# Performance work log

Measured on AMD Instinct MI355X. Metric: run time of the kernel, lower is better.

## Reference

```python
import jax, jax.numpy as jnp
import numpy as np

N_NODES = 50000
N_EDGES = 800000
N_RELS = 20
N_BASES = 8


def setup_inputs() -> dict:
    key = jax.random.key(0)
    ks = jax.random.split(key, 12)
    s = 0.05  # keep activations well-scaled through summed messages
    return {
        "src": jax.random.randint(ks[0], (N_EDGES,), 0, N_NODES),
        "dst": jax.random.randint(ks[1], (N_EDGES,), 0, N_NODES),
        "etype": jax.random.randint(ks[2], (N_EDGES,), 0, N_RELS),
        "num_nodes": N_NODES,
        "basis0": jax.random.normal(ks[3], (N_BASES, 1, 128), jnp.float32) * s,
        "wcomp0": jax.random.normal(ks[4], (N_RELS, N_BASES), jnp.float32),
        "bias0": jax.random.normal(ks[5], (128,), jnp.float32) * s,
        "basis1": jax.random.normal(ks[6], (N_BASES, 128, 128), jnp.float32) * s,
        "wcomp1": jax.random.normal(ks[7], (N_RELS, N_BASES), jnp.float32),
        "bias1": jax.random.normal(ks[8], (128,), jnp.float32) * s,
        "lin_w": jax.random.normal(ks[9], (128, 64), jnp.float32) * s,
        "lin_b": jax.random.normal(ks[10], (64,), jnp.float32) * s,
    }


def _relgraphconv(h, basis, w_comp, bias, src, dst, etype, num_nodes, relu):
    # Basis decomposition: W[r] = sum_b w_comp[r,b] * basis[b]  -> [R, in, out]
    W = jnp.einsum("rb,bio->rio", w_comp, basis)
    # Project every node under every relation once: [N, R, out]
    proj = jnp.einsum("ni,rio->nro", h, W)
    # Per-edge message = h[src] @ W[etype]  (gather, irregular access)
    msg = proj[src, etype]                       # [E, out]
    # Sum-aggregate messages into destination nodes (DGL fn.sum)
    agg = jax.ops.segment_sum(msg, dst, num_segments=num_nodes)
    out = agg + bias
    return jax.nn.relu(out) if relu else out


def reference(src, dst, etype, num_nodes, basis0, wcomp0, bias0,
              basis1, wcomp1, bias1, lin_w, lin_b):
    # Embedder.forward: h starts as ones [N, 1]
    h = jnp.ones((num_nodes, 1), jnp.float32)
    h = _relgraphconv(h, basis0, wcomp0, bias0, src, dst, etype, num_nodes, True)
    h = _relgraphconv(h, basis1, wcomp1, bias1, src, dst, etype, num_nodes, True)
    # conv_output=False -> final layer is plain Linear
    return h @ lin_w + lin_b
```

## Files before the change

### kernel.cpp

```cpp
#include <hip/hip_runtime.h>
#include <hip/hip_bf16.h>

#define NN 50000
#define NE 800000
#define NR 20
#define NB 8
#define D  128
#define DO 64
#define NT 782
#define NBKT (NT*1280)
#define NSB 978

typedef __attribute__((ext_vector_type(8))) short short8;
typedef __attribute__((ext_vector_type(4))) float f32x4;

__device__ inline unsigned short f2bf(float f) {
    __hip_bfloat16 h = __float2bfloat16(f);
    return *reinterpret_cast<unsigned short*>(&h);
}
__device__ inline float bf2f(unsigned short u) {
    unsigned x = ((unsigned)u) << 16;
    float f;
    __builtin_memcpy(&f, &x, 4);
    return f;
}


__global__ __launch_bounds__(1024) void k_wh(
        const int* __restrict__ dst, const int* __restrict__ et,
        const float* __restrict__ basis0, const float* __restrict__ wcomp0,
        const float* __restrict__ basis1, const float* __restrict__ wcomp1,
        const float* __restrict__ lin_w,
        int* __restrict__ cnt2, float* __restrict__ W0,
        unsigned short* __restrict__ W1b, unsigned short* __restrict__ linWb) {
    int b = blockIdx.x;
    if (b < NT) {
        int i = b * 1024 + threadIdx.x;
        if (i < NE) {
            int d = dst[i];
            int key = (d >> 6) * 1280 + et[i] * 64 + (d & 63);
            atomicAdd(&cnt2[key], 1);
        }
        return;
    }
    int idx = (b - NT) * 1024 + threadIdx.x;
    if (idx < NR * D) {
        int r = idx / D, o = idx % D;
        float a = 0.f;
        #pragma unroll
        for (int bb = 0; bb < NB; bb++) a += wcomp0[r * NB + bb] * basis0[bb * D + o];
        W0[idx] = a;
    }
    if (idx < 16 * 64) {
        int lane = idx & 63, fr = idx >> 6;
        int kc = fr >> 2, nt = fr & 3;
        int i0 = kc * 32 + (lane >> 4) * 8;
        int o = nt * 16 + (lane & 15);
        short8 v;
        #pragma unroll
        for (int e = 0; e < 8; e++) v[e] = (short)f2bf(lin_w[(i0 + e) * DO + o]);
        *((short8*)linWb + idx) = v;
    }
    if (idx < NR * 4 * 8 * 64) {
        int lane = idx & 63;
        int cb   = (idx >> 6) & 7;
        int kc   = (idx >> 9) & 3;
        int rel  = idx >> 11;
        float wc[NB];
        #pragma unroll
        for (int bb = 0; bb < NB; bb++) wc[bb] = wcomp1[rel * NB + bb];
        int o  = cb * 16 + (lane & 15);
        int i0 = kc * 32 + (lane >> 4) * 8;
        short8 v;
        #pragma unroll
        for (int e = 0; e < 8; e++) {
            int i = i0 + e;
            float a = 0.f;
            #pragma unroll
            for (int bb = 0; bb < NB; bb++) a += wc[bb] * basis1[(bb * D + i) * D + o];
            v[e] = (short)f2bf(a);
        }
        *((short8*)W1b + idx) = v;
    }
}

__global__ __launch_bounds__(1024) void k_scan1(const int* __restrict__ cnt2,
                                                int* __restrict__ boff2,
                                                int* __restrict__ bsum) {
    __shared__ int ws[16];
    int t = threadIdx.x, lane = t & 63, wv = t >> 6;
    int i = blockIdx.x * 1024 + t;
    int v = (i < NBKT) ? cnt2[i] : 0;
    int inc = v;
    for (int dd = 1; dd < 64; dd <<= 1) {
        int u = __shfl_up(inc, dd);
        if (lane >= dd) inc += u;
    }
    if (lane == 63) ws[wv] = inc;
    __syncthreads();
    if (t == 0) { int a = 0; for (int j = 0; j < 16; j++) { int x = ws[j]; ws[j] = a; a += x; } }
    __syncthreads();
    int ex = ws[wv] + inc - v;
    if (i < NBKT) boff2[i] = ex;
    if (t == 1023) bsum[blockIdx.x] = ex + v;
}

__global__ __launch_bounds__(1024) void k_scan2(int* __restrict__ bsum) {
    __shared__ int ws[16];
    int t = threadIdx.x, lane = t & 63, wv = t >> 6;
    int v = (t < NSB) ? bsum[t] : 0;
    int inc = v;
    for (int dd = 1; dd < 64; dd <<= 1) {
        int u = __shfl_up(inc, dd);
        if (lane >= dd) inc += u;
    }
    if (lane == 63) ws[wv] = inc;
    __syncthreads();
    if (t == 0) { int a = 0; for (int j = 0; j < 16; j++) { int x = ws[j]; ws[j] = a; a += x; } }
    __syncthreads();
    if (t < NSB) bsum[t] = ws[wv] + inc - v;
}

__global__ __launch_bounds__(1024) void k_scan3(int* __restrict__ boff2,
                                                const int* __restrict__ bsum,
                                                int* __restrict__ gcur2) {
    int i = blockIdx.x * 1024 + threadIdx.x;
    if (i < NBKT) {
        int f = boff2[i] + bsum[i >> 10];
        boff2[i] = f;
        gcur2[i] = f;
    }
    if (i == 0) boff2[NBKT] = NE;
}

__global__ __launch_bounds__(1024) void k_sh(
        const int* __restrict__ src, const int* __restrict__ dst,
        const int* __restrict__ et, int* __restrict__ gcur2,
        unsigned short* __restrict__ epack,
        const int* __restrict__ cnt2, const float* __restrict__ W0,
        const float* __restrict__ bias0, unsigned short* __restrict__ h1b) {
    int b = blockIdx.x, t = threadIdx.x;
    if (b < NT) {
        int i = b * 1024 + t;
        if (i < NE) {
            int d = dst[i];
            int key = (d >> 6) * 1280 + et[i] * 64 + (d & 63);
            int pos = atomicAdd(&gcur2[key], 1);
            epack[pos] = (unsigned short)src[i];
        }
        return;
    }
    __shared__ float cs[NR * 64];
    __shared__ float w0s[NR * D];
    int tile = b - NT;
    for (int j = t; j < NR * 64; j += 1024) cs[j] = (float)cnt2[tile * 1280 + j];
    for (int j = t; j < NR * D; j += 1024) w0s[j] = W0[j];
    __syncthreads();
    int nl = t >> 4, cg = t & 15;
    int n = tile * 64 + nl;
    if (n < NN) {
        float a[8];
        #pragma unroll
        for (int j = 0; j < 8; j++) a[j] = bias0[cg * 8 + j];
        for (int r = 0; r < NR; r++) {
            float c = cs[r * 64 + nl];
            #pragma unroll
            for (int j = 0; j < 8; j++) a[j] += c * w0s[r * D + cg * 8 + j];
        }
        short8 o;
        #pragma unroll
        for (int j = 0; j < 8; j++) o[j] = (short)f2bf(fmaxf(a[j], 0.f));
        *((short8*)(h1b + n * D + cg * 8)) = o;
    }
}

__global__ __launch_bounds__(512, 2) void k_mega(
        const unsigned short* __restrict__ epack, const int* __restrict__ boff2,
        const unsigned short* __restrict__ h1b,
        const unsigned short* __restrict__ W1b,
        const unsigned short* __restrict__ linWb,
        const float* __restrict__ bias1, const float* __restrict__ lin_b,
        float* __restrict__ out) {
    __shared__ __align__(16) char lds[17408 + 16384];
    __shared__ unsigned short ooffs[1282];
    __shared__ unsigned short epk[2048];

    short8* Raw8 = (short8*)lds;
    short8* Sl8  = (short8*)(lds + 17408);

    int t = threadIdx.x, tile = blockIdx.x;
    int wv = t >> 6, lane = t & 63;
    int le = t >> 3, lp = t & 7;
    int dl = t >> 3, cg = t & 7;
    int row = lane & 15, gg = lane >> 4;

    int kbase = tile * 1280;
    int tb = boff2[kbase];
    for (int i = t; i < 1281; i += 512)
        ooffs[i] = (unsigned short)(boff2[kbase + i] - tb);
    __syncthreads();
    int nE = min((int)ooffs[1280], 2048);
    for (int i = t; i < nE; i += 512) epk[i] = epack[tb + i];
    __syncthreads();

    f32x4 acc[4];
    #pragma unroll
    for (int j = 0; j < 4; j++) acc[j] = (f32x4){0.f, 0.f, 0.f, 0.f};

    for (int r = 0; r < NR; r++) {
        int rbase = ooffs[r * 64];
        int cnt = ooffs[r * 64 + 64] - rbase;
        if (cnt == 0) continue;

        const short8* Wg8 = (const short8*)W1b + r * 2048;
        short8 breg[4];
        #pragma unroll
        for (int kc = 0; kc < 4; kc++) breg[kc] = Wg8[(kc * 8 + wv) * 64 + lane];

        float s[16];
        #pragma unroll
        for (int k = 0; k < 16; k++) s[k] = 0.f;
        int o0 = ooffs[r * 64 + dl] - rbase;
        int o1 = ooffs[r * 64 + dl + 1] - rbase;
        int nc = (cnt + 63) >> 6;

        for (int c = 0; c < nc; c++) {
            int cb0 = c * 64, m = min(64, cnt - cb0);
            if (c > 0) __syncthreads();
            if (le < m) {
                int node = epk[rbase + cb0 + le];
                const short8* hp = (const short8*)(h1b + (size_t)node * D) + lp * 2;
                Raw8[le * 17 + lp * 2]     = hp[0];
                Raw8[le * 17 + lp * 2 + 1] = hp[1];
            }
            __syncthreads();
            int lo = max(o0 - cb0, 0), hi = min(o1 - cb0, m);
            for (int p = lo; p < hi; p++) {
                short8 w0 = Raw8[p * 17 + 2 * cg];
                short8 w1 = Raw8[p * 17 + 2 * cg + 1];
                #pragma unroll
                for (int k = 0; k < 8; k++) {
                    s[k]     += bf2f((unsigned short)w0[k]);
                    s[8 + k] += bf2f((unsigned short)w1[k]);
                }
            }
        }
        short8 p0, p1;
        #pragma unroll
        for (int k = 0; k < 8; k++) {
            p0[k] = (short)f2bf(s[k]);
            p1[k] = (short)f2bf(s[8 + k]);
        }
        Sl8[dl * 16 + ((cg * 2)     ^ (dl & 15))] = p0;
        Sl8[dl * 16 + ((cg * 2 + 1) ^ (dl & 15))] = p1;
        __syncthreads();
        #pragma unroll
        for (int rb = 0; rb < 4; rb++) {
            int arow = rb * 16 + row;
            #pragma unroll
            for (int kc = 0; kc < 4; kc++) {
                short8 a = Sl8[arow * 16 + ((kc * 4 + gg) ^ (arow & 15))];
                acc[rb] = __builtin_amdgcn_mfma_f32_16x16x32_bf16(a, breg[kc], acc[rb], 0, 0, 0);
            }
        }
    }

    __syncthreads();
    unsigned short* Af = (unsigned short*)lds;
    #pragma unroll
    for (int rb = 0; rb < 4; rb++) {
        #pragma unroll
        for (int reg = 0; reg < 4; reg++) {
            int rr = rb * 16 + gg * 4 + reg;
            int col = wv * 16 + row;
            Af[rr * 136 + col] = f2bf(fmaxf(acc[rb][reg] + bias1[col], 0.f));
        }
    }
    __syncthreads();
    {
        int rb = wv & 3;
        int nt0 = (wv >> 2) * 2, nt1 = nt0 + 1;
        f32x4 ao0 = (f32x4){0.f, 0.f, 0.f, 0.f};
        f32x4 ao1 = (f32x4){0.f, 0.f, 0.f, 0.f};
        #pragma unroll
        for (int kc = 0; kc < 4; kc++) {
            short8 a = *(const short8*)(Af + (rb * 16 + row) * 136 + kc * 32 + gg * 8);
            short8 b0 = *((const short8*)linWb + (kc * 4 + nt0) * 64 + lane);
            short8 b1 = *((const short8*)linWb + (kc * 4 + nt1) * 64 + lane);
            ao0 = __builtin_amdgcn_mfma_f32_16x16x32_bf16(a, b0, ao0, 0, 0, 0);
            ao1 = __builtin_amdgcn_mfma_f32_16x16x32_bf16(a, b1, ao1, 0, 0, 0);
        }
        float lb0 = lin_b[nt0 * 16 + row];
        float lb1 = lin_b[nt1 * 16 + row];
        #pragma unroll
        for (int reg = 0; reg < 4; reg++) {
            int d = tile * 64 + rb * 16 + gg * 4 + reg;
            if (d < NN) {
                out[d * DO + nt0 * 16 + row] = ao0[reg] + lb0;
                out[d * DO + nt1 * 16 + row] = ao1[reg] + lb1;
            }
        }
    }
}

extern "C" void kernel_launch(void* const* d_in, const int* in_sizes, int n_in,
                              void* d_out, int out_size, void* d_ws, size_t ws_size,
                              hipStream_t stream) {
    const int*   src    = (const int*)d_in[0];
    const int*   dst    = (const int*)d_in[1];
    const int*   et     = (const int*)d_in[2];
    const float* basis0 = (const float*)d_in[4];
    const float* wcomp0 = (const float*)d_in[5];
    const float* bias0  = (const float*)d_in[6];
    const float* basis1 = (const float*)d_in[7];
    const float* wcomp1 = (const float*)d_in[8];
    const float* bias1  = (const float*)d_in[9];
    const float* lin_w  = (const float*)d_in[10];
    const float* lin_b  = (const float*)d_in[11];
    float* out = (float*)d_out;

    char* ws = (char*)d_ws;
    int*            cnt2    = (int*)           (ws + 0);
    int*            bsum    = (int*)           (ws + 4003840);
    int*            boff2   = (int*)           (ws + 4007808);
    int*            gcur2   = (int*)           (ws + 8011712);
    float*          W0      = (float*)         (ws + 12015616);
    unsigned short* W1b     = (unsigned short*)(ws + 12025856);
    unsigned short* h1b     = (unsigned short*)(ws + 12681216);
    unsigned short* epack   = (unsigned short*)(ws + 25481216);
    unsigned short* linWb   = (unsigned short*)(ws + 28681216);

    hipMemsetAsync(ws, 0, 4003840, stream);

    k_wh<<<NT + 40, 1024, 0, stream>>>(dst, et, basis0, wcomp0, basis1, wcomp1,
                                       lin_w, cnt2, W0, W1b, linWb);
    k_scan1<<<NSB, 1024, 0, stream>>>(cnt2, boff2, bsum);
    k_scan2<<<1, 1024, 0, stream>>>(bsum);
    k_scan3<<<NSB, 1024, 0, stream>>>(boff2, bsum, gcur2);
    k_sh<<<NT * 2, 1024, 0, stream>>>(src, dst, et, gcur2, epack,
                                      cnt2, W0, bias0, h1b);
    k_mega<<<NT, 512, 0, stream>>>(epack, boff2, h1b, W1b, linWb,
                                   bias1, lin_b, out);
}
```

Before: 190.0 us.

## Replace fine-grained global bucket scan with coarse tile-relation scan plus in-LDS sub-sort

The global counting sort now buckets edges by (dst tile, relation) instead of (dst tile, relation, dst lane). This shrinks the scan to a single-block kernel and drops two scan launches. Each edge packs relation, local dst and src into one int, and the mega kernel re-sorts its tile's edges in LDS using per-tile counts and local atomics. The aim is to cut scan work, kernel launches and the memset size, at the cost of extra LDS atomics, a per-block local scan, and 4-byte rather than 2-byte edge records.

```diff
diff --git a/kernel.cpp b/kernel.cpp
--- a/kernel.cpp
+++ b/kernel.cpp
@@ -8,8 +8,7 @@
 #define D  128
 #define DO 64
 #define NT 782
-#define NBKT (NT*1280)
-#define NSB 978
+#define NRB (NT*NR)
 
 typedef __attribute__((ext_vector_type(8))) short short8;
 typedef __attribute__((ext_vector_type(4))) float f32x4;
@@ -31,15 +30,16 @@
         const float* __restrict__ basis0, const float* __restrict__ wcomp0,
         const float* __restrict__ basis1, const float* __restrict__ wcomp1,
         const float* __restrict__ lin_w,
-        int* __restrict__ cnt2, float* __restrict__ W0,
-        unsigned short* __restrict__ W1b, unsigned short* __restrict__ linWb) {
+        int* __restrict__ cnt2, int* __restrict__ cntR,
+        float* __restrict__ W0, unsigned short* __restrict__ W1b,
+        unsigned short* __restrict__ linWb) {
     int b = blockIdx.x;
     if (b < NT) {
         int i = b * 1024 + threadIdx.x;
         if (i < NE) {
-            int d = dst[i];
-            int key = (d >> 6) * 1280 + et[i] * 64 + (d & 63);
-            atomicAdd(&cnt2[key], 1);
+            int d = dst[i], e = et[i];
+            atomicAdd(&cnt2[(d >> 6) * 1280 + e * 64 + (d & 63)], 1);
+            atomicAdd(&cntR[(d >> 6) * NR + e], 1);
         }
         return;
     }
@@ -84,69 +84,50 @@
     }
 }
 
-__global__ __launch_bounds__(1024) void k_scan1(const int* __restrict__ cnt2,
-                                                int* __restrict__ boff2,
-                                                int* __restrict__ bsum) {
+__global__ __launch_bounds__(1024) void k_scanR(const int* __restrict__ cntR,
+                                                int* __restrict__ boffR,
+                                                int* __restrict__ gcurR) {
     __shared__ int ws[16];
     int t = threadIdx.x, lane = t & 63, wv = t >> 6;
-    int i = blockIdx.x * 1024 + t;
-    int v = (i < NBKT) ? cnt2[i] : 0;
-    int inc = v;
+    int v[16]; int s = 0;
+    #pragma unroll
+    for (int j = 0; j < 16; j++) {
+        int idx = t * 16 + j;
+        v[j] = (idx < NRB) ? cntR[idx] : 0;
+        s += v[j];
+    }
+    int inc = s;
     for (int dd = 1; dd < 64; dd <<= 1) {
         int u = __shfl_up(inc, dd);
         if (lane >= dd) inc += u;
     }
     if (lane == 63) ws[wv] = inc;
     __syncthreads();
-    if (t == 0) { int a = 0; for (int j = 0; j < 16; j++) { int x = ws[j]; ws[j] = a; a += x; } }
-    __syncthreads();
-    int ex = ws[wv] + inc - v;
-    if (i < NBKT) boff2[i] = ex;
-    if (t == 1023) bsum[blockIdx.x] = ex + v;
-}
-
-__global__ __launch_bounds__(1024) void k_scan2(int* __restrict__ bsum) {
-    __shared__ int ws[16];
-    int t = threadIdx.x, lane = t & 63, wv = t >> 6;
-    int v = (t < NSB) ? bsum[t] : 0;
-    int inc = v;
-    for (int dd = 1; dd < 64; dd <<= 1) {
-        int u = __shfl_up(inc, dd);
-        if (lane >= dd) inc += u;
-    }
-    if (lane == 63) ws[wv] = inc;
-    __syncthreads();
-    if (t == 0) { int a = 0; for (int j = 0; j < 16; j++) { int x = ws[j]; ws[j] = a; a += x; } }
-    __syncthreads();
-    if (t < NSB) bsum[t] = ws[wv] + inc - v;
-}
-
-__global__ __launch_bounds__(1024) void k_scan3(int* __restrict__ boff2,
-                                                const int* __restrict__ bsum,
-                                                int* __restrict__ gcur2) {
-    int i = blockIdx.x * 1024 + threadIdx.x;
-    if (i < NBKT) {
-        int f = boff2[i] + bsum[i >> 10];
-        boff2[i] = f;
-        gcur2[i] = f;
-    }
-    if (i == 0) boff2[NBKT] = NE;
+    if (t == 0) { int a = 0; for (int i = 0; i < 16; i++) { int x = ws[i]; ws[i] = a; a += x; } }
+    __syncthreads();
+    int base = ws[wv] + inc - s;
+    #pragma unroll
+    for (int j = 0; j < 16; j++) {
+        int idx = t * 16 + j;
+        if (idx < NRB) { boffR[idx] = base; gcurR[idx] = base; }
+        base += v[j];
+    }
+    if (t == 1023) boffR[NRB] = base;
 }
 
 __global__ __launch_bounds__(1024) void k_sh(
         const int* __restrict__ src, const int* __restrict__ dst,
-        const int* __restrict__ et, int* __restrict__ gcur2,
-        unsigned short* __restrict__ epack,
+        const int* __restrict__ et, int* __restrict__ gcurR,
+        int* __restrict__ epack2,
         const int* __restrict__ cnt2, const float* __restrict__ W0,
         const float* __restrict__ bias0, unsigned short* __restrict__ h1b) {
     int b = blockIdx.x, t = threadIdx.x;
     if (b < NT) {
         int i = b * 1024 + t;
         if (i < NE) {
-            int d = dst[i];
-            int key = (d >> 6) * 1280 + et[i] * 64 + (d & 63);
-            int pos = atomicAdd(&gcur2[key], 1);
-            epack[pos] = (unsigned short)src[i];
+            int d = dst[i], e = et[i];
+            int pos = atomicAdd(&gcurR[(d >> 6) * NR + e], 1);
+            epack2[pos] = (e << 22) | ((d & 63) << 16) | src[i];
         }
         return;
     }
@@ -175,7 +156,8 @@
 }
 
 __global__ __launch_bounds__(512, 2) void k_mega(
-        const unsigned short* __restrict__ epack, const int* __restrict__ boff2,
+        const int* __restrict__ epack2, const int* __restrict__ boffR,
+        const int* __restrict__ cnt2,
         const unsigned short* __restrict__ h1b,
         const unsigned short* __restrict__ W1b,
         const unsigned short* __restrict__ linWb,
@@ -184,9 +166,12 @@
     __shared__ __align__(16) char lds[17408 + 16384];
     __shared__ unsigned short ooffs[1282];
     __shared__ unsigned short epk[2048];
+    __shared__ int swsc[8];
 
     short8* Raw8 = (short8*)lds;
     short8* Sl8  = (short8*)(lds + 17408);
+    int* stag = (int*)lds;
+    int* lcur = (int*)(lds + 17408);
 
     int t = threadIdx.x, tile = blockIdx.x;
     int wv = t >> 6, lane = t & 63;
@@ -194,13 +179,38 @@
     int dl = t >> 3, cg = t & 7;
     int row = lane & 15, gg = lane >> 4;
 
-    int kbase = tile * 1280;
-    int tb = boff2[kbase];
-    for (int i = t; i < 1281; i += 512)
-        ooffs[i] = (unsigned short)(boff2[kbase + i] - tb);
-    __syncthreads();
-    int nE = min((int)ooffs[1280], 2048);
-    for (int i = t; i < nE; i += 512) epk[i] = epack[tb + i];
+    int tb = boffR[tile * NR];
+    int b3 = t * 3;
+    int c0 = (b3     < 1280) ? cnt2[tile * 1280 + b3]     : 0;
+    int c1 = (b3 + 1 < 1280) ? cnt2[tile * 1280 + b3 + 1] : 0;
+    int c2 = (b3 + 2 < 1280) ? cnt2[tile * 1280 + b3 + 2] : 0;
+    int s3 = c0 + c1 + c2;
+    int inc = s3;
+    for (int dd = 1; dd < 64; dd <<= 1) {
+        int u = __shfl_up(inc, dd);
+        if (lane >= dd) inc += u;
+    }
+    if (lane == 63) swsc[wv] = inc;
+    __syncthreads();
+    if (t == 0) { int a = 0; for (int j = 0; j < 8; j++) { int x = swsc[j]; swsc[j] = a; a += x; } }
+    __syncthreads();
+    int base = swsc[wv] + inc - s3;
+    if (b3     < 1280) ooffs[b3]     = (unsigned short)base;
+    if (b3 + 1 < 1280) ooffs[b3 + 1] = (unsigned short)(base + c0);
+    if (b3 + 2 < 1280) ooffs[b3 + 2] = (unsigned short)(base + c0 + c1);
+    if (t == 511) ooffs[1280] = (unsigned short)(base + s3);
+    __syncthreads();
+
+    int cntT = min((int)ooffs[1280], 2048);
+    for (int i = t; i < 1280; i += 512) lcur[i] = ooffs[i];
+    for (int j = t; j < cntT; j += 512) stag[j] = epack2[tb + j];
+    __syncthreads();
+    for (int j = t; j < cntT; j += 512) {
+        int e = stag[j];
+        int key = ((e >> 22) & 31) * 64 + ((e >> 16) & 63);
+        int pos = atomicAdd(&lcur[key], 1);
+        if (pos < 2048) epk[pos] = (unsigned short)(e & 0xFFFF);
+    }
     __syncthreads();
 
     f32x4 acc[4];
@@ -320,25 +330,23 @@
     float* out = (float*)d_out;
 
     char* ws = (char*)d_ws;
-    int*            cnt2    = (int*)           (ws + 0);
-    int*            bsum    = (int*)           (ws + 4003840);
-    int*            boff2   = (int*)           (ws + 4007808);
-    int*            gcur2   = (int*)           (ws + 8011712);
-    float*          W0      = (float*)         (ws + 12015616);
-    unsigned short* W1b     = (unsigned short*)(ws + 12025856);
-    unsigned short* h1b     = (unsigned short*)(ws + 12681216);
-    unsigned short* epack   = (unsigned short*)(ws + 25481216);
-    unsigned short* linWb   = (unsigned short*)(ws + 28681216);
-
-    hipMemsetAsync(ws, 0, 4003840, stream);
+    int*            cnt2   = (int*)           (ws + 0);
+    int*            cntR   = (int*)           (ws + 4003840);
+    int*            boffR  = (int*)           (ws + 4066432);
+    int*            gcurR  = (int*)           (ws + 4129024);
+    float*          W0     = (float*)         (ws + 4191616);
+    unsigned short* W1b    = (unsigned short*)(ws + 4201856);
+    unsigned short* h1b    = (unsigned short*)(ws + 4857216);
+    int*            epack2 = (int*)           (ws + 17657216);
+    unsigned short* linWb  = (unsigned short*)(ws + 20857216);
+
+    hipMemsetAsync(ws, 0, 4066400, stream);
 
     k_wh<<<NT + 40, 1024, 0, stream>>>(dst, et, basis0, wcomp0, basis1, wcomp1,
-                                       lin_w, cnt2, W0, W1b, linWb);
-    k_scan1<<<NSB, 1024, 0, stream>>>(cnt2, boff2, bsum);
-    k_scan2<<<1, 1024, 0, stream>>>(bsum);
-    k_scan3<<<NSB, 1024, 0, stream>>>(boff2, bsum, gcur2);
-    k_sh<<<NT * 2, 1024, 0, stream>>>(src, dst, et, gcur2, epack,
+                                       lin_w, cnt2, cntR, W0, W1b, linWb);
+    k_scanR<<<1, 1024, 0, stream>>>(cntR, boffR, gcurR);
+    k_sh<<<NT * 2, 1024, 0, stream>>>(src, dst, et, gcurR, epack2,
                                       cnt2, W0, bias0, h1b);
-    k_mega<<<NT, 512, 0, stream>>>(epack, boff2, h1b, W1b, linWb,
+    k_mega<<<NT, 512, 0, stream>>>(epack2, boffR, cnt2, h1b, W1b, linWb,
                                    bias1, lin_b, out);
 }
```

Result: slower. 231.5 us (+21.8%).

## Merge three-kernel scan into single-pass scan with last-block block-sum fixup

Applied to the files above, without the earlier changes.

Replaces the scan1/scan2/scan3 chain with one kernel. Each block writes local exclusive offsets, and the last block to finish, found through an atomic counter, scans the per-block sums. Consumers (k_sh scatter and k_mega offsets) add the block prefix bsum[key>>10] on the fly instead of relying on a separate fixup pass. This removes two kernel launches and one full pass over the bucket array, at the cost of extra indexed loads in the consumers. The boff2[NBKT] sentinel now holds the local prefix, which is corrected by adding bpre.

```diff
diff --git a/kernel.cpp b/kernel.cpp
--- a/kernel.cpp
+++ b/kernel.cpp
@@ -86,8 +86,11 @@
 
 __global__ __launch_bounds__(1024) void k_scan1(const int* __restrict__ cnt2,
                                                 int* __restrict__ boff2,
-                                                int* __restrict__ bsum) {
+                                                int* __restrict__ gcur2,
+                                                int* __restrict__ bsum,
+                                                int* __restrict__ scancnt) {
     __shared__ int ws[16];
+    __shared__ int lastf;
     int t = threadIdx.x, lane = t & 63, wv = t >> 6;
     int i = blockIdx.x * 1024 + t;
     int v = (i < NBKT) ? cnt2[i] : 0;
@@ -101,41 +104,34 @@
     if (t == 0) { int a = 0; for (int j = 0; j < 16; j++) { int x = ws[j]; ws[j] = a; a += x; } }
     __syncthreads();
     int ex = ws[wv] + inc - v;
-    if (i < NBKT) boff2[i] = ex;
-    if (t == 1023) bsum[blockIdx.x] = ex + v;
-}
-
-__global__ __launch_bounds__(1024) void k_scan2(int* __restrict__ bsum) {
-    __shared__ int ws[16];
-    int t = threadIdx.x, lane = t & 63, wv = t >> 6;
-    int v = (t < NSB) ? bsum[t] : 0;
-    int inc = v;
+    if (i < NBKT) { boff2[i] = ex; gcur2[i] = ex; }
+    if (i == NBKT) boff2[NBKT] = ex;
+    if (t == 1023) {
+        bsum[blockIdx.x] = ex + v;
+        __threadfence();
+        int done = atomicAdd(scancnt, 1);
+        lastf = (done == (int)gridDim.x - 1);
+    }
+    __syncthreads();
+    if (!lastf) return;
+    int v2 = (t < NSB) ? atomicAdd(&bsum[t], 0) : 0;
+    int inc2 = v2;
     for (int dd = 1; dd < 64; dd <<= 1) {
-        int u = __shfl_up(inc, dd);
-        if (lane >= dd) inc += u;
-    }
-    if (lane == 63) ws[wv] = inc;
+        int u = __shfl_up(inc2, dd);
+        if (lane >= dd) inc2 += u;
+    }
+    __syncthreads();
+    if (lane == 63) ws[wv] = inc2;
     __syncthreads();
     if (t == 0) { int a = 0; for (int j = 0; j < 16; j++) { int x = ws[j]; ws[j] = a; a += x; } }
     __syncthreads();
-    if (t < NSB) bsum[t] = ws[wv] + inc - v;
-}
-
-__global__ __launch_bounds__(1024) void k_scan3(int* __restrict__ boff2,
-                                                const int* __restrict__ bsum,
-                                                int* __restrict__ gcur2) {
-    int i = blockIdx.x * 1024 + threadIdx.x;
-    if (i < NBKT) {
-        int f = boff2[i] + bsum[i >> 10];
-        boff2[i] = f;
-        gcur2[i] = f;
-    }
-    if (i == 0) boff2[NBKT] = NE;
+    if (t < NSB) bsum[t] = ws[wv] + inc2 - v2;
 }
 
 __global__ __launch_bounds__(1024) void k_sh(
         const int* __restrict__ src, const int* __restrict__ dst,
         const int* __restrict__ et, int* __restrict__ gcur2,
+        const int* __restrict__ bpre,
         unsigned short* __restrict__ epack,
         const int* __restrict__ cnt2, const float* __restrict__ W0,
         const float* __restrict__ bias0, unsigned short* __restrict__ h1b) {
@@ -146,7 +142,7 @@
             int d = dst[i];
             int key = (d >> 6) * 1280 + et[i] * 64 + (d & 63);
             int pos = atomicAdd(&gcur2[key], 1);
-            epack[pos] = (unsigned short)src[i];
+            epack[pos + bpre[key >> 10]] = (unsigned short)src[i];
         }
         return;
     }
@@ -176,6 +172,7 @@
 
 __global__ __launch_bounds__(512, 2) void k_mega(
         const unsigned short* __restrict__ epack, const int* __restrict__ boff2,
+        const int* __restrict__ bpre,
         const unsigned short* __restrict__ h1b,
         const unsigned short* __restrict__ W1b,
         const unsigned short* __restrict__ linWb,
@@ -195,12 +192,14 @@
     int row = lane & 15, gg = lane >> 4;
 
     int kbase = tile * 1280;
-    int tb = boff2[kbase];
-    for (int i = t; i < 1281; i += 512)
-        ooffs[i] = (unsigned short)(boff2[kbase + i] - tb);
+    int tbg = boff2[kbase] + bpre[kbase >> 10];
+    for (int i = t; i < 1281; i += 512) {
+        int gi = kbase + i;
+        ooffs[i] = (unsigned short)(boff2[gi] + bpre[gi >> 10] - tbg);
+    }
     __syncthreads();
     int nE = min((int)ooffs[1280], 2048);
-    for (int i = t; i < nE; i += 512) epk[i] = epack[tb + i];
+    for (int i = t; i < nE; i += 512) epk[i] = epack[tbg + i];
     __syncthreads();
 
     f32x4 acc[4];
@@ -322,6 +321,7 @@
     char* ws = (char*)d_ws;
     int*            cnt2    = (int*)           (ws + 0);
     int*            bsum    = (int*)           (ws + 4003840);
+    int*            scancnt = (int*)           (ws + 4007752);
     int*            boff2   = (int*)           (ws + 4007808);
     int*            gcur2   = (int*)           (ws + 8011712);
     float*          W0      = (float*)         (ws + 12015616);
@@ -330,15 +330,13 @@
     unsigned short* epack   = (unsigned short*)(ws + 25481216);
     unsigned short* linWb   = (unsigned short*)(ws + 28681216);
 
-    hipMemsetAsync(ws, 0, 4003840, stream);
+    hipMemsetAsync(ws, 0, 4007756, stream);
 
     k_wh<<<NT + 40, 1024, 0, stream>>>(dst, et, basis0, wcomp0, basis1, wcomp1,
                                        lin_w, cnt2, W0, W1b, linWb);
-    k_scan1<<<NSB, 1024, 0, stream>>>(cnt2, boff2, bsum);
-    k_scan2<<<1, 1024, 0, stream>>>(bsum);
-    k_scan3<<<NSB, 1024, 0, stream>>>(boff2, bsum, gcur2);
-    k_sh<<<NT * 2, 1024, 0, stream>>>(src, dst, et, gcur2, epack,
+    k_scan1<<<NSB, 1024, 0, stream>>>(cnt2, boff2, gcur2, bsum, scancnt);
+    k_sh<<<NT * 2, 1024, 0, stream>>>(src, dst, et, gcur2, bsum, epack,
                                       cnt2, W0, bias0, h1b);
-    k_mega<<<NT, 512, 0, stream>>>(epack, boff2, h1b, W1b, linWb,
+    k_mega<<<NT, 512, 0, stream>>>(epack, boff2, bsum, h1b, W1b, linWb,
                                    bias1, lin_b, out);
 }
```

After: 215.7 us. +13.5%, slower.
